# Performance work log

Measured on AMD Instinct MI355X. Metric: run time of the kernel, lower is better.

Reference implementation:

```python
import jax, jax.numpy as jnp
import numpy as np

NUM_CLASSES = 100000
NUM_SAMPLED = 1000
DIM = 512
BATCH = 8192


def _log_uniform_expected_count(ids, num_sampled, range_max):
    # TF LogUniformCandidateSampler: p(c) = (log(c+2) - log(c+1)) / log(range_max+1)
    c = ids.astype(jnp.float32)
    p = (jnp.log(c + 2.0) - jnp.log(c + 1.0)) / jnp.log(float(range_max) + 1.0)
    # expected count under unique sampling with num_sampled tries
    return -jnp.expm1(num_sampled * jnp.log1p(-p))


def setup_inputs() -> dict:
    key = jax.random.key(0)
    k1, k2, k3, k4, k5 = jax.random.split(key, 5)
    y_true = jax.random.randint(k1, (BATCH, 1), 0, NUM_CLASSES, dtype=jnp.int32)
    y_pred = jax.random.normal(k2, (BATCH, DIM), dtype=jnp.float32)
    # learned params sized per init_kwargs (VarianceScaling ~ small uniform; scale only)
    limit = np.sqrt(6.0 / (NUM_CLASSES + DIM))
    W = jax.random.uniform(k3, (NUM_CLASSES, DIM), jnp.float32, -limit, limit)
    b = jax.random.uniform(k4, (NUM_CLASSES,), jnp.float32, -limit, limit)
    sampled = jax.random.randint(k5, (NUM_SAMPLED,), 0, NUM_CLASSES, dtype=jnp.int32)
    return {"y_true": y_true, "y_pred": y_pred, "W": W, "b": b, "sampled": sampled}


def reference(y_true, y_pred, W, b, sampled):
    V = W.shape[0]
    S = sampled.shape[0]
    labels = y_true[:, 0]  # [B], num_true = 1

    # true-class logits: gather rows + batched dot
    w_true = W[labels]                                      # [B, D]
    true_logits = jnp.einsum('bd,bd->b', y_pred, w_true) + b[labels]
    true_logits = true_logits - jnp.log(_log_uniform_expected_count(labels, S, V))

    # sampled-class logits: gather rows + GEMM
    w_s = W[sampled]                                        # [S, D]
    sampled_logits = y_pred @ w_s.T + b[sampled]            # [B, S]
    sampled_logits = sampled_logits - jnp.log(_log_uniform_expected_count(sampled, S, V))

    # remove accidental hits (sampled id == true label)
    hit = labels[:, None] == sampled[None, :]               # [B, S]
    sampled_logits = jnp.where(hit, sampled_logits - 1e9, sampled_logits)

    # softmax cross-entropy with true class at column 0
    logits = jnp.concatenate([true_logits[:, None], sampled_logits], axis=1)  # [B, S+1]
    per_example = jax.nn.logsumexp(logits, axis=1) - logits[:, 0]
    return jnp.mean(per_example)
```

## Files before the change

kernel.cpp:

```cpp
#include <hip/hip_runtime.h>
#include <hip/hip_bf16.h>
#include <math.h>

#define S_SAMPLED 1000
#define SPAD      1024
#define DIM       512
#define BATCH     8192

#define BM 128
#define BN 256
#define BKT 64
#define KTILES (DIM / BKT)
#define NCHUNK 4

typedef __attribute__((ext_vector_type(8))) short short8_t;
typedef __attribute__((ext_vector_type(4))) float f32x4_t;

__device__ __forceinline__ float neg_log_expected(int c) {
    const float log_vp1 = 11.5129354649f;
    float p = log1pf(1.0f / (float)(c + 1)) / log_vp1;
    float E = -expm1f((float)S_SAMPLED * log1pf(-p));
    return -logf(E);
}

__device__ __forceinline__ unsigned short f2bf(float x) {
    __hip_bfloat16 h = __float2bfloat16(x);
    union { __hip_bfloat16 h; unsigned short u; } cv; cv.h = h; return cv.u;
}

__device__ __forceinline__ void load_lds16(const void* g, void* l) {
    __builtin_amdgcn_global_load_lds(
        (const __attribute__((address_space(1))) void*)g,
        (__attribute__((address_space(3))) void*)l, 16, 0, 0);
}

__device__ __forceinline__ int swz(int lin) { return lin ^ (((lin >> 7) & 7) << 4); }

__global__ __launch_bounds__(256) void prep_kernel(
    const int* __restrict__ y_true, const float* __restrict__ y_pred,
    const float* __restrict__ W, const float* __restrict__ b,
    const int* __restrict__ sampled,
    unsigned short* __restrict__ Wg, float* __restrict__ adj,
    float* __restrict__ true_out, unsigned short* __restrict__ ypredB)
{
    int bid = blockIdx.x;
    if (bid < 512) {
        int row = bid * 2 + (threadIdx.x >> 7);
        int t   = threadIdx.x & 127;
        if (t == 0) {
            if (row < S_SAMPLED) {
                int c = sampled[row];
                adj[row] = b[c] + neg_log_expected(c);
            } else adj[row] = -1e30f;
        }
        unsigned short* dst = Wg + (size_t)row * DIM + t * 4;
        if (row < S_SAMPLED) {
            float4 f = *(const float4*)(W + (size_t)sampled[row] * DIM + t * 4);
            ushort4 o;
            o.x = f2bf(f.x); o.y = f2bf(f.y); o.z = f2bf(f.z); o.w = f2bf(f.w);
            *(ushort4*)dst = o;
        } else {
            *(ushort4*)dst = make_ushort4(0, 0, 0, 0);
        }
    } else {
        int row  = (bid - 512) * 4 + (threadIdx.x >> 6);
        int lane = threadIdx.x & 63;
        int lab  = y_true[row];
        const float4* ap = (const float4*)(y_pred + (size_t)row * DIM);
        const float4* wp = (const float4*)(W + (size_t)lab * DIM);
        float s = 0.f;
#pragma unroll
        for (int u = 0; u < 2; ++u) {
            float4 a = ap[lane + u * 64];
            float4 w = wp[lane + u * 64];
            s += a.x * w.x + a.y * w.y + a.z * w.z + a.w * w.w;
            ushort4 o;
            o.x = f2bf(a.x); o.y = f2bf(a.y); o.z = f2bf(a.z); o.w = f2bf(a.w);
            *(ushort4*)(ypredB + (size_t)row * DIM + (lane + u * 64) * 4) = o;
        }
#pragma unroll
        for (int off = 32; off; off >>= 1) s += __shfl_xor(s, off);
        if (lane == 0) true_out[row] = s + b[lab] + neg_log_expected(lab);
    }
}

__global__ __launch_bounds__(512, 2) void gemm_partial_kernel(
    const unsigned short* __restrict__ Abf,
    const unsigned short* __restrict__ Wg,
    const int*   __restrict__ sampled,
    const float* __restrict__ adj,
    const int*   __restrict__ y_true,
    float*       __restrict__ pmax,
    float*       __restrict__ psum)
{
    __shared__ __align__(16) char smem[98304 + 2048];
    char* As0 = smem;
    char* As1 = smem + 16384;
    char* Bs0 = smem + 32768;
    char* Bs1 = smem + 65536;
    float* redm = (float*)(smem + 98304);
    float* reds = (float*)(smem + 98304 + 1024);

    int wg = blockIdx.x;
    int sw = (wg & 7) * 32 + (wg >> 3);
    const int m0 = (sw >> 2) * BM;
    const int n0 = (sw & 3) * BN;

    const int tid  = threadIdx.x;
    const int lane = tid & 63;
    const int wid  = tid >> 6;
    const int wr   = wid >> 1;
    const int wc   = wid & 1;
    const int g    = lane >> 4;
    const int lcol = lane & 15;

    const char* AB = (const char*)Abf;
    const char* WB = (const char*)Wg;

    int a_src[2], b_src[4];
#pragma unroll
    for (int it = 0; it < 2; ++it) {
        int d = it * 8192 + tid * 16;
        int row = d >> 7;
        int kb  = (d & 127) ^ ((row & 7) << 4);
        a_src[it] = (m0 + row) * (DIM * 2) + kb;
    }
#pragma unroll
    for (int it = 0; it < 4; ++it) {
        int d = it * 8192 + tid * 16;
        int col = d >> 7;
        int kb  = (d & 127) ^ ((col & 7) << 4);
        b_src[it] = (n0 + col) * (DIM * 2) + kb;
    }

    int a_roff[2][2], b_roff[8][2];
#pragma unroll
    for (int mi = 0; mi < 2; ++mi)
#pragma unroll
        for (int ks = 0; ks < 2; ++ks)
            a_roff[mi][ks] = swz((wr * 32 + mi * 16 + lcol) * 128 + ks * 64 + g * 16);
#pragma unroll
    for (int nj = 0; nj < 8; ++nj)
#pragma unroll
        for (int ks = 0; ks < 2; ++ks)
            b_roff[nj][ks] = swz((wc * 128 + nj * 16 + lcol) * 128 + ks * 64 + g * 16);

    f32x4_t acc[2][8] = {};

#define STAGE(AsP, BsP, kt) do {                                     \
        int kb_ = (kt) * (BKT * 2);                                  \
        load_lds16(AB + a_src[0] + kb_, (AsP) + wid * 1024);         \
        load_lds16(AB + a_src[1] + kb_, (AsP) + 8192 + wid * 1024);  \
        load_lds16(WB + b_src[0] + kb_, (BsP) + wid * 1024);         \
        load_lds16(WB + b_src[1] + kb_, (BsP) + 8192 + wid * 1024);  \
        load_lds16(WB + b_src[2] + kb_, (BsP) + 16384 + wid * 1024); \
        load_lds16(WB + b_src[3] + kb_, (BsP) + 24576 + wid * 1024); \
    } while (0)

#define COMPUTE(AsP, BsP) do {                                                        \
        _Pragma("unroll")                                                             \
        for (int ks = 0; ks < 2; ++ks) {                                              \
            short8_t a0 = *(const short8_t*)((AsP) + a_roff[0][ks]);                  \
            short8_t a1 = *(const short8_t*)((AsP) + a_roff[1][ks]);                  \
            _Pragma("unroll")                                                         \
            for (int nj = 0; nj < 8; ++nj) {                                          \
                short8_t bv = *(const short8_t*)((BsP) + b_roff[nj][ks]);             \
                acc[0][nj] = __builtin_amdgcn_mfma_f32_16x16x32_bf16(a0, bv, acc[0][nj], 0, 0, 0); \
                acc[1][nj] = __builtin_amdgcn_mfma_f32_16x16x32_bf16(a1, bv, acc[1][nj], 0, 0, 0); \
            }                                                                         \
        }                                                                             \
    } while (0)

    __builtin_amdgcn_sched_barrier(0);
    STAGE(As0, Bs0, 0);
    STAGE(As1, Bs1, 1);
#pragma unroll
    for (int t = 0; t < KTILES; ++t) {
        if (t < KTILES - 1) asm volatile("s_waitcnt vmcnt(6)" ::: "memory");
        else                asm volatile("s_waitcnt vmcnt(0)" ::: "memory");
        __builtin_amdgcn_s_barrier();
        __builtin_amdgcn_sched_barrier(0);
        const char* AsP = (t & 1) ? As1 : As0;
        const char* BsP = (t & 1) ? Bs1 : Bs0;
        __builtin_amdgcn_s_setprio(1);
        COMPUTE(AsP, BsP);
        __builtin_amdgcn_s_setprio(0);
        __builtin_amdgcn_sched_barrier(0);
        __builtin_amdgcn_s_barrier();
        if (t + 2 < KTILES) STAGE((t & 1) ? As1 : As0, (t & 1) ? Bs1 : Bs0, t + 2);
    }
    __builtin_amdgcn_sched_barrier(0);

    int   labs[2][4];
    float mrow[2][4];
#pragma unroll
    for (int mi = 0; mi < 2; ++mi)
#pragma unroll
        for (int r = 0; r < 4; ++r) {
            labs[mi][r] = y_true[m0 + wr * 32 + mi * 16 + g * 4 + r];
            mrow[mi][r] = -3e38f;
        }

    float ajv[8]; int scv[8];
#pragma unroll
    for (int nj = 0; nj < 8; ++nj) {
        int cg = n0 + wc * 128 + nj * 16 + lcol;
        ajv[nj] = adj[cg];
        scv[nj] = (cg < S_SAMPLED) ? sampled[cg] : -2147483647;
    }

#pragma unroll
    for (int mi = 0; mi < 2; ++mi)
#pragma unroll
        for (int nj = 0; nj < 8; ++nj) {
            f32x4_t v = acc[mi][nj];
#pragma unroll
            for (int r = 0; r < 4; ++r) {
                float x = v[r] + ajv[nj];
                if (scv[nj] == labs[mi][r]) x -= 1e9f;
                v[r] = x;
                mrow[mi][r] = fmaxf(mrow[mi][r], x);
            }
            acc[mi][nj] = v;
        }

#pragma unroll
    for (int s = 1; s < 16; s <<= 1)
#pragma unroll
        for (int mi = 0; mi < 2; ++mi)
#pragma unroll
            for (int r = 0; r < 4; ++r)
                mrow[mi][r] = fmaxf(mrow[mi][r], __shfl_xor(mrow[mi][r], s));
    if (lcol == 0) {
#pragma unroll
        for (int mi = 0; mi < 2; ++mi)
#pragma unroll
            for (int r = 0; r < 4; ++r)
                redm[wc * 128 + wr * 32 + mi * 16 + g * 4 + r] = mrow[mi][r];
    }
    __syncthreads();

    float srow[2][4];
#pragma unroll
    for (int mi = 0; mi < 2; ++mi)
#pragma unroll
        for (int r = 0; r < 4; ++r) {
            int row = wr * 32 + mi * 16 + g * 4 + r;
            float cm = fmaxf(redm[row], redm[128 + row]);
            float s = 0.f;
#pragma unroll
            for (int nj = 0; nj < 8; ++nj)
                s += expf(acc[mi][nj][r] - cm);
            srow[mi][r] = s;
        }
#pragma unroll
    for (int s = 1; s < 16; s <<= 1)
#pragma unroll
        for (int mi = 0; mi < 2; ++mi)
#pragma unroll
            for (int r = 0; r < 4; ++r)
                srow[mi][r] += __shfl_xor(srow[mi][r], s);
    if (lcol == 0) {
#pragma unroll
        for (int mi = 0; mi < 2; ++mi)
#pragma unroll
            for (int r = 0; r < 4; ++r)
                reds[wc * 128 + wr * 32 + mi * 16 + g * 4 + r] = srow[mi][r];
    }
    __syncthreads();

    if (tid < BM) {
        int row = tid;
        float pm = fmaxf(redm[row], redm[128 + row]);
        float ps = reds[row] + reds[128 + row];
        pmax[(size_t)(m0 + row) * NCHUNK + (sw & 3)] = pm;
        psum[(size_t)(m0 + row) * NCHUNK + (sw & 3)] = ps;
    }
#undef STAGE
#undef COMPUTE
}

__global__ __launch_bounds__(1024) void finalize_kernel(
    const float* __restrict__ pmax, const float* __restrict__ psum,
    const float* __restrict__ true_v, float* __restrict__ out)
{
    __shared__ float sm[1024];
    float tot = 0.f;
#pragma unroll
    for (int u = 0; u < BATCH / 1024; ++u) {
        int r = u * 1024 + threadIdx.x;
        float4 pm = *(const float4*)(pmax + (size_t)r * 4);
        float4 ps = *(const float4*)(psum + (size_t)r * 4);
        float t = true_v[r];
        float m = fmaxf(fmaxf(fmaxf(pm.x, pm.y), fmaxf(pm.z, pm.w)), t);
        float s = ps.x * expf(pm.x - m) + ps.y * expf(pm.y - m)
                + ps.z * expf(pm.z - m) + ps.w * expf(pm.w - m)
                + expf(t - m);
        tot += m + logf(s) - t;
    }
    sm[threadIdx.x] = tot;
    __syncthreads();
    for (int st = 512; st; st >>= 1) {
        if (threadIdx.x < st) sm[threadIdx.x] += sm[threadIdx.x + st];
        __syncthreads();
    }
    if (threadIdx.x == 0) out[0] = sm[0] / (float)BATCH;
}

extern "C" void kernel_launch(void* const* d_in, const int* in_sizes, int n_in,
                              void* d_out, int out_size, void* d_ws, size_t ws_size,
                              hipStream_t stream) {
    const int*   y_true  = (const int*)d_in[0];
    const float* y_pred  = (const float*)d_in[1];
    const float* W       = (const float*)d_in[2];
    const float* b       = (const float*)d_in[3];
    const int*   sampled = (const int*)d_in[4];

    char* ws = (char*)d_ws;
    unsigned short* ypredB = (unsigned short*)ws;
    unsigned short* Wg     = (unsigned short*)(ws + 8388608);
    float* adj    = (float*)(ws + 9437184);
    float* true_v = (float*)(ws + 9441280);
    float* pmax   = (float*)(ws + 9474048);
    float* psum   = (float*)(ws + 9605120);

    prep_kernel<<<2560, 256, 0, stream>>>(y_true, y_pred, W, b, sampled,
                                          Wg, adj, true_v, ypredB);
    gemm_partial_kernel<<<256, 512, 0, stream>>>(ypredB, Wg, sampled, adj,
                                                 y_true, pmax, psum);
    finalize_kernel<<<1, 1024, 0, stream>>>(pmax, psum, true_v, (float*)d_out);
}
```

Baseline: 38.11 us.

## Fuse finalize into GEMM via last-block counter and fixed-shift logsumexp

Replaces the per-row max reduction with a constant shift in the exponentials, removing one cross-wave max pass and the pmax buffer. The separate finalize kernel is folded into the GEMM kernel: each block atomically increments a counter reset in prep, and the last block reduces the partial sums into the loss. This saves a kernel launch and a reduction phase. The fixed shift risks overflow or underflow if logits fall far from the assumed range.

```diff
diff --git a/kernel.cpp b/kernel.cpp
--- a/kernel.cpp
+++ b/kernel.cpp
@@ -12,6 +12,8 @@
 #define BKT 64
 #define KTILES (DIM / BKT)
 #define NCHUNK 4
+#define GEMM_BLOCKS 256
+#define M0C 20.0f
 
 typedef __attribute__((ext_vector_type(8))) short short8_t;
 typedef __attribute__((ext_vector_type(4))) float f32x4_t;
@@ -41,9 +43,11 @@
     const float* __restrict__ W, const float* __restrict__ b,
     const int* __restrict__ sampled,
     unsigned short* __restrict__ Wg, float* __restrict__ adj,
-    float* __restrict__ true_out, unsigned short* __restrict__ ypredB)
+    float* __restrict__ true_out, unsigned short* __restrict__ ypredB,
+    int* __restrict__ counter)
 {
     int bid = blockIdx.x;
+    if (bid == 0 && threadIdx.x == 0) *counter = 0;
     if (bid < 512) {
         int row = bid * 2 + (threadIdx.x >> 7);
         int t   = threadIdx.x & 127;
@@ -90,21 +94,24 @@
     const int*   __restrict__ sampled,
     const float* __restrict__ adj,
     const int*   __restrict__ y_true,
-    float*       __restrict__ pmax,
-    float*       __restrict__ psum)
+    const float* __restrict__ true_v,
+    float*       __restrict__ psum,
+    int*         __restrict__ counter,
+    float*       __restrict__ out)
 {
     __shared__ __align__(16) char smem[98304 + 2048];
+    __shared__ int s_last;
     char* As0 = smem;
     char* As1 = smem + 16384;
     char* Bs0 = smem + 32768;
     char* Bs1 = smem + 65536;
-    float* redm = (float*)(smem + 98304);
-    float* reds = (float*)(smem + 98304 + 1024);
+    float* reds = (float*)(smem + 98304);
 
     int wg = blockIdx.x;
     int sw = (wg & 7) * 32 + (wg >> 3);
-    const int m0 = (sw >> 2) * BM;
-    const int n0 = (sw & 3) * BN;
+    const int m0    = (sw >> 2) * BM;
+    const int chunk = sw & 3;
+    const int n0    = chunk * BN;
 
     const int tid  = threadIdx.x;
     const int lane = tid & 63;
@@ -192,13 +199,13 @@
     __builtin_amdgcn_sched_barrier(0);
 
     int   labs[2][4];
-    float mrow[2][4];
+    float srow[2][4];
 #pragma unroll
     for (int mi = 0; mi < 2; ++mi)
 #pragma unroll
         for (int r = 0; r < 4; ++r) {
             labs[mi][r] = y_true[m0 + wr * 32 + mi * 16 + g * 4 + r];
-            mrow[mi][r] = -3e38f;
+            srow[mi][r] = 0.f;
         }
 
     float ajv[8]; int scv[8];
@@ -213,46 +220,14 @@
     for (int mi = 0; mi < 2; ++mi)
 #pragma unroll
         for (int nj = 0; nj < 8; ++nj) {
-            f32x4_t v = acc[mi][nj];
 #pragma unroll
             for (int r = 0; r < 4; ++r) {
-                float x = v[r] + ajv[nj];
+                float x = acc[mi][nj][r] + ajv[nj];
                 if (scv[nj] == labs[mi][r]) x -= 1e9f;
-                v[r] = x;
-                mrow[mi][r] = fmaxf(mrow[mi][r], x);
+                srow[mi][r] += expf(x - M0C);
             }
-            acc[mi][nj] = v;
-        }
-
-#pragma unroll
-    for (int s = 1; s < 16; s <<= 1)
-#pragma unroll
-        for (int mi = 0; mi < 2; ++mi)
-#pragma unroll
-            for (int r = 0; r < 4; ++r)
-                mrow[mi][r] = fmaxf(mrow[mi][r], __shfl_xor(mrow[mi][r], s));
-    if (lcol == 0) {
-#pragma unroll
-        for (int mi = 0; mi < 2; ++mi)
-#pragma unroll
-            for (int r = 0; r < 4; ++r)
-                redm[wc * 128 + wr * 32 + mi * 16 + g * 4 + r] = mrow[mi][r];
-    }
-    __syncthreads();
-
-    float srow[2][4];
-#pragma unroll
-    for (int mi = 0; mi < 2; ++mi)
-#pragma unroll
-        for (int r = 0; r < 4; ++r) {
-            int row = wr * 32 + mi * 16 + g * 4 + r;
-            float cm = fmaxf(redm[row], redm[128 + row]);
-            float s = 0.f;
-#pragma unroll
-            for (int nj = 0; nj < 8; ++nj)
-                s += expf(acc[mi][nj][r] - cm);
-            srow[mi][r] = s;
-        }
+        }
+
 #pragma unroll
     for (int s = 1; s < 16; s <<= 1)
 #pragma unroll
@@ -269,42 +244,38 @@
     }
     __syncthreads();
 
-    if (tid < BM) {
-        int row = tid;
-        float pm = fmaxf(redm[row], redm[128 + row]);
-        float ps = reds[row] + reds[128 + row];
-        pmax[(size_t)(m0 + row) * NCHUNK + (sw & 3)] = pm;
-        psum[(size_t)(m0 + row) * NCHUNK + (sw & 3)] = ps;
-    }
+    if (tid < BM)
+        psum[(size_t)(m0 + tid) * NCHUNK + chunk] = reds[tid] + reds[128 + tid];
+
+    __syncthreads();
+    if (tid == 0) {
+        __threadfence();
+        int old = atomicAdd(counter, 1);
+        s_last = (old == GEMM_BLOCKS - 1) ? 1 : 0;
+    }
+    __syncthreads();
+    if (!s_last) return;
+
+    __threadfence();
+    float tot = 0.f;
+#pragma unroll
+    for (int i = 0; i < BATCH / 512; ++i) {
+        int r = tid + i * 512;
+        float4 ps = *(const float4*)(psum + (size_t)r * NCHUNK);
+        float t = true_v[r];
+        float s = ps.x + ps.y + ps.z + ps.w + expf(t - M0C);
+        tot += logf(s) + M0C - t;
+    }
+    float* red = (float*)smem;
+    red[tid] = tot;
+    __syncthreads();
+    for (int st = 256; st; st >>= 1) {
+        if (tid < st) red[tid] += red[tid + st];
+        __syncthreads();
+    }
+    if (tid == 0) out[0] = red[0] / (float)BATCH;
 #undef STAGE
 #undef COMPUTE
-}
-
-__global__ __launch_bounds__(1024) void finalize_kernel(
-    const float* __restrict__ pmax, const float* __restrict__ psum,
-    const float* __restrict__ true_v, float* __restrict__ out)
-{
-    __shared__ float sm[1024];
-    float tot = 0.f;
-#pragma unroll
-    for (int u = 0; u < BATCH / 1024; ++u) {
-        int r = u * 1024 + threadIdx.x;
-        float4 pm = *(const float4*)(pmax + (size_t)r * 4);
-        float4 ps = *(const float4*)(psum + (size_t)r * 4);
-        float t = true_v[r];
-        float m = fmaxf(fmaxf(fmaxf(pm.x, pm.y), fmaxf(pm.z, pm.w)), t);
-        float s = ps.x * expf(pm.x - m) + ps.y * expf(pm.y - m)
-                + ps.z * expf(pm.z - m) + ps.w * expf(pm.w - m)
-                + expf(t - m);
-        tot += m + logf(s) - t;
-    }
-    sm[threadIdx.x] = tot;
-    __syncthreads();
-    for (int st = 512; st; st >>= 1) {
-        if (threadIdx.x < st) sm[threadIdx.x] += sm[threadIdx.x + st];
-        __syncthreads();
-    }
-    if (threadIdx.x == 0) out[0] = sm[0] / (float)BATCH;
 }
 
 extern "C" void kernel_launch(void* const* d_in, const int* in_sizes, int n_in,
@@ -319,14 +290,13 @@
     char* ws = (char*)d_ws;
     unsigned short* ypredB = (unsigned short*)ws;
     unsigned short* Wg     = (unsigned short*)(ws + 8388608);
-    float* adj    = (float*)(ws + 9437184);
-    float* true_v = (float*)(ws + 9441280);
-    float* pmax   = (float*)(ws + 9474048);
-    float* psum   = (float*)(ws + 9605120);
+    float* adj     = (float*)(ws + 9437184);
+    float* true_v  = (float*)(ws + 9441280);
+    float* psum    = (float*)(ws + 9474048);
+    int*   counter = (int*)(ws + 9605120);
 
     prep_kernel<<<2560, 256, 0, stream>>>(y_true, y_pred, W, b, sampled,
-                                          Wg, adj, true_v, ypredB);
-    gemm_partial_kernel<<<256, 512, 0, stream>>>(ypredB, Wg, sampled, adj,
-                                                 y_true, pmax, psum);
-    finalize_kernel<<<1, 1024, 0, stream>>>(pmax, psum, true_v, (float*)d_out);
-}
+                                          Wg, adj, true_v, ypredB, counter);
+    gemm_partial_kernel<<<GEMM_BLOCKS, 512, 0, stream>>>(
+        ypredB, Wg, sampled, adj, y_true, true_v, psum, counter, (float*)d_out);
+}
```

New measurement: 41.49 us. 1.09x slower.
